# Kernel tuning notes

Measured on AMD Instinct MI355X. Metric: run time of the kernel, lower is better.

Reference implementation:

```python
import jax, jax.numpy as jnp
import numpy as np

B, L, D, H, DH, DEPTH, VOCAB = 8, 512, 256, 8, 64, 16, 5
INNER = 4 * D  # GLU feedforward inner dim = 1024
EPS = 1e-5

def _ln(x, g, b):
    mu = jnp.mean(x, -1, keepdims=True)
    var = jnp.mean(jnp.square(x - mu), -1, keepdims=True)
    return (x - mu) * jax.lax.rsqrt(var + EPS) * g + b

def setup_inputs() -> dict:
    key = jax.random.key(0)
    ks = jax.random.split(key, 24)
    s = 0.02
    seq = jax.random.randint(ks[0], (B, L), 0, VOCAB)
    lengths = jax.random.randint(ks[1], (B,), L // 2, L + 1)
    mask = jnp.arange(L)[None, :] < lengths[:, None]  # [B, L] bool padding mask
    f32 = jnp.float32
    return {
        "seq": seq,
        "mask": mask,
        "emb": jax.random.normal(ks[2], (VOCAB, D), f32) * s,
        "png": jnp.ones((D,), f32), "pnb": jnp.zeros((D,), f32),
        "ln1g": jnp.ones((DEPTH, D), f32), "ln1b": jnp.zeros((DEPTH, D), f32),
        "Wq": jax.random.normal(ks[3], (DEPTH, D, H * DH), f32) * s,
        "Wk": jax.random.normal(ks[4], (DEPTH, D, H * DH), f32) * s,
        "Wv": jax.random.normal(ks[5], (DEPTH, D, H * DH), f32) * s,
        "Wo": jax.random.normal(ks[6], (DEPTH, H * DH, D), f32) * s,
        "ln2g": jnp.ones((DEPTH, D), f32), "ln2b": jnp.zeros((DEPTH, D), f32),
        "W1": jax.random.normal(ks[7], (DEPTH, D, 2 * INNER), f32) * s,
        "b1": jnp.zeros((DEPTH, 2 * INNER), f32),
        "W2": jax.random.normal(ks[8], (DEPTH, INNER, D), f32) * s,
        "b2": jnp.zeros((DEPTH, D), f32),
        "fng": jnp.ones((D,), f32), "fnb": jnp.zeros((D,), f32),
        "Wout": jax.random.normal(ks[9], (D, 2), f32) * s,
        "bout": jnp.zeros((2,), f32),
    }

def _alibi_bias(n):
    # heads=8 is a power of two: slopes = 2^{-1}..2^{-8}
    slopes = 2.0 ** (-(jnp.arange(1, H + 1, dtype=jnp.float32)) * (8.0 / H))
    pos = jnp.arange(n, dtype=jnp.float32)
    rel = -jnp.abs(pos[None, :] - pos[:, None])  # [n, n]
    return slopes[:, None, None] * rel  # [H, n, n]

def _forward(seq, mask, emb, png, pnb, ln1g, ln1b, Wq, Wk, Wv, Wo,
             ln2g, ln2b, W1, b1, W2, b2, fng, fnb, Wout, bout):
    x = emb[seq]                      # [B, L, D]
    x = _ln(x, png, pnb)              # post_emb_norm
    bias = _alibi_bias(L)             # [H, L, L]
    kv_mask = mask[:, None, None, :]  # [B, 1, 1, L]
    scale = DH ** -0.5

    def layer(x, p):
        (g1, c1, wq, wk, wv, wo, g2, c2, w1, bb1, w2, bb2) = p
        h = _ln(x, g1, c1)
        q = (h @ wq).reshape(B, L, H, DH).transpose(0, 2, 1, 3)  # bhld
        k = (h @ wk).reshape(B, L, H, DH).transpose(0, 2, 1, 3)
        v = (h @ wv).reshape(B, L, H, DH).transpose(0, 2, 1, 3)
        scores = jnp.einsum('bhid,bhjd->bhij', q, k) * scale + bias
        scores = jnp.where(kv_mask, scores, jnp.float32(-1e9))
        a = jax.nn.softmax(scores, axis=-1)
        o = jnp.einsum('bhij,bhjd->bhid', a, v)
        o = o.transpose(0, 2, 1, 3).reshape(B, L, H * DH) @ wo
        x = x + o
        h2 = _ln(x, g2, c2)
        u = h2 @ w1 + bb1
        val, gate = jnp.split(u, 2, axis=-1)  # GLU: x * gelu(gate)
        x = x + (val * jax.nn.gelu(gate, approximate=False)) @ w2 + bb2
        return x, None

    x, _ = jax.lax.scan(layer, x, (ln1g, ln1b, Wq, Wk, Wv, Wo, ln2g, ln2b, W1, b1, W2, b2))
    x = _ln(x, fng, fnb)              # final encoder norm
    return x @ Wout + bout            # [B, L, 2]

def reference(seq, mask, emb, png, pnb, ln1g, ln1b, Wq, Wk, Wv, Wo,
              ln2g, ln2b, W1, b1, W2, b2, fng, fnb, Wout, bout):
    return _forward(seq, mask, emb, png, pnb, ln1g, ln1b, Wq, Wk, Wv, Wo,
                    ln2g, ln2b, W1, b1, W2, b2, fng, fnb, Wout, bout)
```

## Files before the change

kernel.cpp:

```cpp
#include <hip/hip_runtime.h>
#include <cstdint>
#include <cstddef>

#define BB 8
#define LL 512
#define DD 256
#define HH 8
#define DHD 64
#define NLAYER 16
#define HDH 512
#define IN2 2048
#define IN1 1024

typedef __attribute__((ext_vector_type(8))) short short8;
typedef __attribute__((ext_vector_type(4))) float floatx4;
typedef __attribute__((ext_vector_type(4))) unsigned short ushort4v;
typedef unsigned short u16;

__device__ __forceinline__ floatx4 mfma16(short8 a, short8 b, floatx4 c) {
  return __builtin_amdgcn_mfma_f32_16x16x32_bf16(a, b, c, 0, 0, 0);
}

__device__ __forceinline__ u16 f2b(float f) {
  union { float f; unsigned u; } x; x.f = f;
  unsigned u = x.u + 0x7fffu + ((x.u >> 16) & 1u);
  return (u16)(u >> 16);
}
__device__ __forceinline__ float b2f(u16 s) {
  union { unsigned u; float f; } x; x.u = ((unsigned)s) << 16;
  return x.f;
}

__device__ __forceinline__ float wave_sum(float s) {
#pragma unroll
  for (int off = 32; off; off >>= 1) s += __shfl_xor(s, off);
  return s;
}

__device__ __forceinline__ void gload_lds16(const u16* g, u16* l) {
  __builtin_amdgcn_global_load_lds((__attribute__((address_space(1))) void*)g,
                                   (__attribute__((address_space(3))) void*)l,
                                   16, 0, 0);
}

template <int NSLOTS, int NTHREADS = 256>
__device__ __forceinline__ void stage_tile(const u16* __restrict__ g, int rowstride,
                                           u16* lds, int tid) {
  int wave = tid >> 6, lane = tid & 63;
#pragma unroll
  for (int j = 0; j < NSLOTS / NTHREADS; ++j) {
    int sbase = j * NTHREADS + wave * 64;
    int slot = sbase + lane;
    int row = slot >> 3;
    int kg = (slot & 7) ^ (row & 7);
    gload_lds16(g + (size_t)row * rowstride + kg * 8, lds + sbase * 8);
  }
}

__device__ __forceinline__ short8 ld_frag(const u16* T, int row, int kg) {
  return *(const short8*)&T[(row << 6) + (((kg ^ row) & 7) << 3)];
}

__device__ __forceinline__ float4 ln_math(const float* __restrict__ x,
                                          const float* __restrict__ g,
                                          const float* __restrict__ b, int t) {
  float4 v = *(const float4*)(x + t * 4);
  float s = wave_sum(v.x + v.y + v.z + v.w);
  float mu = s * (1.0f / DD);
  float dx = v.x - mu, dy = v.y - mu, dz = v.z - mu, dw = v.w - mu;
  float ss = wave_sum(dx * dx + dy * dy + dz * dz + dw * dw);
  float r = rsqrtf(ss * (1.0f / DD) + 1e-5f);
  float4 gg = *(const float4*)(g + t * 4);
  float4 bb = *(const float4*)(b + t * 4);
  float4 o;
  o.x = dx * r * gg.x + bb.x;
  o.y = dy * r * gg.y + bb.y;
  o.z = dz * r * gg.z + bb.z;
  o.w = dw * r * gg.w + bb.w;
  return o;
}

__global__ __launch_bounds__(256) void embed_ln_kernel(
    const int* __restrict__ seq, const float* __restrict__ emb,
    const float* __restrict__ png, const float* __restrict__ pnb,
    const float* __restrict__ g1, const float* __restrict__ b1,
    float* __restrict__ X, u16* __restrict__ H) {
  int row = blockIdx.x * 4 + (threadIdx.x >> 6), t = threadIdx.x & 63;
  int tok = seq[row];
  float4 o = ln_math(emb + (size_t)tok * DD, png, pnb, t);
  *(float4*)(X + (size_t)row * DD + t * 4) = o;
  float s = wave_sum(o.x + o.y + o.z + o.w);
  float mu = s * (1.0f / DD);
  float dx = o.x - mu, dy = o.y - mu, dz = o.z - mu, dw = o.w - mu;
  float ss = wave_sum(dx * dx + dy * dy + dz * dz + dw * dw);
  float r = rsqrtf(ss * (1.0f / DD) + 1e-5f);
  float4 gg = *(const float4*)(g1 + t * 4);
  float4 bb = *(const float4*)(b1 + t * 4);
  ushort4v o4;
  o4[0] = f2b(dx * r * gg.x + bb.x);
  o4[1] = f2b(dy * r * gg.y + bb.y);
  o4[2] = f2b(dz * r * gg.z + bb.z);
  o4[3] = f2b(dw * r * gg.w + bb.w);
  *(ushort4v*)(H + (size_t)row * DD + t * 4) = o4;
}

#define WBUF_LAYER 1310720
__global__ __launch_bounds__(256) void prep_weights_kernel(
    const float* __restrict__ Wq, const float* __restrict__ Wk,
    const float* __restrict__ Wv, const float* __restrict__ Wo,
    const float* __restrict__ W1, const float* __restrict__ W2,
    u16* __restrict__ wbuf_all) {
  __shared__ float tile[32][33];
  int l = blockIdx.x / 1280;
  int bx = blockIdx.x % 1280;
  int tid = threadIdx.x;
  const float* wq = Wq + (size_t)l * DD * HDH;
  const float* wk = Wk + (size_t)l * DD * HDH;
  const float* wv = Wv + (size_t)l * DD * HDH;
  const float* wo = Wo + (size_t)l * HDH * DD;
  const float* w1 = W1 + (size_t)l * DD * IN2;
  const float* w2 = W2 + (size_t)l * IN1 * DD;
  u16* wbuf = wbuf_all + (size_t)l * WBUF_LAYER;

  const float* src; int srcld; u16* dst; int dstld; int dn0, k0, scol0;
  int packW1 = 0;
  if (bx < 384) {
    int t = bx; dn0 = (t % 48) * 32; k0 = (t / 48) * 32;
    scol0 = dn0 & 511;
    src = (dn0 < 512) ? wq : ((dn0 < 1024) ? wk : wv);
    srcld = 512; dst = wbuf; dstld = 256;
  } else if (bx < 512) {
    int t = bx - 384; dn0 = (t % 8) * 32; k0 = (t / 8) * 32; scol0 = dn0;
    src = wo; srcld = 256; dst = wbuf + 393216; dstld = 512;
  } else if (bx < 1024) {
    int t = bx - 512; dn0 = (t % 64) * 32; k0 = (t / 64) * 32; scol0 = dn0;
    src = w1; srcld = 2048; dst = wbuf + 524288; dstld = 256; packW1 = 1;
  } else {
    int t = bx - 1024; dn0 = (t % 8) * 32; k0 = (t / 8) * 32; scol0 = dn0;
    src = w2; srcld = 256; dst = wbuf + 1048576; dstld = 1024;
  }
  int r = tid >> 3, c4 = (tid & 7) * 4;
  float4 v = *(const float4*)&src[(size_t)(k0 + r) * srcld + scol0 + c4];
  tile[r][c4 + 0] = v.x; tile[r][c4 + 1] = v.y;
  tile[r][c4 + 2] = v.z; tile[r][c4 + 3] = v.w;
  __syncthreads();
  int n = tid >> 3, kk = (tid & 7) * 4;
  int drow = dn0 + n;
  if (packW1) {
    if (drow < 1024) drow = ((drow >> 4) << 5) | (drow & 15);
    else { int nn = drow - 1024; drow = (((nn >> 4) << 5) + 16) | (nn & 15); }
  }
  ushort4v o4;
  o4[0] = f2b(tile[kk + 0][n]); o4[1] = f2b(tile[kk + 1][n]);
  o4[2] = f2b(tile[kk + 2][n]); o4[3] = f2b(tile[kk + 3][n]);
  *(ushort4v*)&dst[(size_t)drow * dstld + k0 + kk] = o4;
}

__global__ __launch_bounds__(256) void gemm_qkv(
    const u16* __restrict__ A, const u16* __restrict__ BT,
    u16* __restrict__ qk, u16* __restrict__ vT) {
  __shared__ __align__(16) u16 As[2][128 * 64];
  __shared__ __align__(16) u16 Bs[2][128 * 64];
  int tid = threadIdx.x;
  int wave = tid >> 6, lane = tid & 63;
  int lm = lane & 15, quad = lane >> 4;
  int wr = wave >> 1, wc = wave & 1;
  int n0 = blockIdx.x * 128, m0 = blockIdx.y * 128;
  const u16* Ab = A + (size_t)m0 * DD;
  const u16* Bb = BT + (size_t)n0 * DD;

  floatx4 acc[4][4];
#pragma unroll
  for (int mf = 0; mf < 4; ++mf)
#pragma unroll
    for (int nf = 0; nf < 4; ++nf)
#pragma unroll
      for (int r = 0; r < 4; ++r) acc[mf][nf][r] = 0.0f;

  stage_tile<1024>(Ab, DD, As[0], tid);
  stage_tile<1024>(Bb, DD, Bs[0], tid);
  __syncthreads();
#pragma unroll
  for (int it = 0; it < 4; ++it) {
    if (it < 3) {
      stage_tile<1024>(Ab + (it + 1) * 64, DD, As[(it + 1) & 1], tid);
      stage_tile<1024>(Bb + (it + 1) * 64, DD, Bs[(it + 1) & 1], tid);
    }
    const u16* Ac = As[it & 1];
    const u16* Bc = Bs[it & 1];
#pragma unroll
    for (int kc = 0; kc < 2; ++kc) {
      short8 af[4], bf[4];
#pragma unroll
      for (int mf = 0; mf < 4; ++mf)
        af[mf] = ld_frag(Ac, wr * 64 + mf * 16 + lm, kc * 4 + quad);
#pragma unroll
      for (int nf = 0; nf < 4; ++nf)
        bf[nf] = ld_frag(Bc, wc * 64 + nf * 16 + lm, kc * 4 + quad);
#pragma unroll
      for (int mf = 0; mf < 4; ++mf)
#pragma unroll
        for (int nf = 0; nf < 4; ++nf)
          acc[mf][nf] = mfma16(af[mf], bf[nf], acc[mf][nf]);
    }
    if (it < 3) __syncthreads();
  }
  if (n0 < 1024) {
#pragma unroll
    for (int mf = 0; mf < 4; ++mf)
#pragma unroll
      for (int nf = 0; nf < 4; ++nf)
#pragma unroll
        for (int r = 0; r < 4; ++r) {
          int row = m0 + wr * 64 + mf * 16 + quad * 4 + r;
          int col = n0 + wc * 64 + nf * 16 + lm;
          qk[(size_t)row * 1024 + col] = f2b(acc[mf][nf][r]);
        }
  } else {
#pragma unroll
    for (int mf = 0; mf < 4; ++mf)
#pragma unroll
      for (int nf = 0; nf < 4; ++nf) {
        int token0 = m0 + wr * 64 + mf * 16 + quad * 4;
        int hd = n0 + wc * 64 + nf * 16 + lm - 1024;
        int b = token0 >> 9, key = token0 & 511;
        ushort4v p4;
#pragma unroll
        for (int r = 0; r < 4; ++r) p4[r] = f2b(acc[mf][nf][r]);
        *(ushort4v*)&vT[((size_t)(b * 8 + (hd >> 6)) * 64 + (hd & 63)) * 512 + key] = p4;
      }
  }
}

__global__ __launch_bounds__(256) void gemm_ffn1(
    const u16* __restrict__ A, const u16* __restrict__ BTp,
    const float* __restrict__ b1, u16* __restrict__ G) {
  __shared__ __align__(16) u16 As[2][128 * 64];
  __shared__ __align__(16) u16 Bs[2][128 * 64];
  int tid = threadIdx.x;
  int wave = tid >> 6, lane = tid & 63;
  int lm = lane & 15, quad = lane >> 4;
  int wr = wave >> 1, wc = wave & 1;
  int n0 = blockIdx.x * 128, m0 = blockIdx.y * 128;
  const u16* Ab = A + (size_t)m0 * DD;
  const u16* Bb = BTp + (size_t)n0 * DD;

  floatx4 acc[4][4];
#pragma unroll
  for (int mf = 0; mf < 4; ++mf)
#pragma unroll
    for (int nf = 0; nf < 4; ++nf)
#pragma unroll
      for (int r = 0; r < 4; ++r) acc[mf][nf][r] = 0.0f;

  stage_tile<1024>(Ab, DD, As[0], tid);
  stage_tile<1024>(Bb, DD, Bs[0], tid);
  __syncthreads();
#pragma unroll
  for (int it = 0; it < 4; ++it) {
    if (it < 3) {
      stage_tile<1024>(Ab + (it + 1) * 64, DD, As[(it + 1) & 1], tid);
      stage_tile<1024>(Bb + (it + 1) * 64, DD, Bs[(it + 1) & 1], tid);
    }
    const u16* Ac = As[it & 1];
    const u16* Bc = Bs[it & 1];
#pragma unroll
    for (int kc = 0; kc < 2; ++kc) {
      short8 af[4], bf[4];
#pragma unroll
      for (int mf = 0; mf < 4; ++mf)
        af[mf] = ld_frag(Ac, wr * 64 + mf * 16 + lm, kc * 4 + quad);
#pragma unroll
      for (int nf = 0; nf < 4; ++nf)
        bf[nf] = ld_frag(Bc, wc * 64 + nf * 16 + lm, kc * 4 + quad);
#pragma unroll
      for (int mf = 0; mf < 4; ++mf)
#pragma unroll
        for (int nf = 0; nf < 4; ++nf)
          acc[mf][nf] = mfma16(af[mf], bf[nf], acc[mf][nf]);
    }
    if (it < 3) __syncthreads();
  }
  int p0 = (n0 + wc * 64) >> 5;
#pragma unroll
  for (int j = 0; j < 2; ++j) {
    int gcol = (p0 + j) * 16 + lm;
    float bv = b1[gcol], bg = b1[1024 + gcol];
#pragma unroll
    for (int mf = 0; mf < 4; ++mf)
#pragma unroll
      for (int r = 0; r < 4; ++r) {
        int row = m0 + wr * 64 + mf * 16 + quad * 4 + r;
        float val = acc[mf][2 * j][r] + bv;
        float gate = acc[mf][2 * j + 1][r] + bg;
        float ge = 0.5f * gate * (1.0f + erff(gate * 0.70710678118654752440f));
        G[(size_t)row * IN1 + gcol] = f2b(val * ge);
      }
  }
}

__global__ __launch_bounds__(512) void gemm_row_ln(
    const u16* __restrict__ A, int lda, const u16* __restrict__ BT, int K,
    const float* __restrict__ bias, float* __restrict__ X,
    const float* __restrict__ lng, const float* __restrict__ lnb,
    u16* __restrict__ Hout,
    const float* __restrict__ Wout, const float* __restrict__ bout,
    float* __restrict__ outp) {
  __shared__ __align__(16) u16 As[2][16 * 64];
  __shared__ __align__(16) u16 Bs[2][256 * 64];
  int tid = threadIdx.x;
  int wave = tid >> 6, lane = tid & 63;
  int lm = lane & 15, quad = lane >> 4;
  int m0 = blockIdx.x * 16;

  floatx4 acc[2];
#pragma unroll
  for (int nf = 0; nf < 2; ++nf)
#pragma unroll
    for (int r = 0; r < 4; ++r) acc[nf][r] = 0.0f;

  const u16* Ab = A + (size_t)m0 * lda;
  if (wave < 2) {
    int slot = wave * 64 + lane;
    int row = slot >> 3, kg = (slot & 7) ^ (row & 7);
    gload_lds16(Ab + (size_t)row * lda + kg * 8, As[0] + wave * 64 * 8);
  }
  stage_tile<2048, 512>(BT, K, Bs[0], tid);
  __syncthreads();
  int iters = K >> 6;
  for (int it = 0; it < iters; ++it) {
    if (it + 1 < iters) {
      int kn = (it + 1) * 64;
      if (wave < 2) {
        int slot = wave * 64 + lane;
        int row = slot >> 3, kg = (slot & 7) ^ (row & 7);
        gload_lds16(Ab + (size_t)row * lda + kn + kg * 8,
                    As[(it + 1) & 1] + wave * 64 * 8);
      }
      stage_tile<2048, 512>(BT + kn, K, Bs[(it + 1) & 1], tid);
    }
    const u16* Ac = As[it & 1];
    const u16* Bc = Bs[it & 1];
#pragma unroll
    for (int kc = 0; kc < 2; ++kc) {
      short8 af = ld_frag(Ac, lm, kc * 4 + quad);
#pragma unroll
      for (int nf = 0; nf < 2; ++nf) {
        short8 bf = ld_frag(Bc, wave * 32 + nf * 16 + lm, kc * 4 + quad);
        acc[nf] = mfma16(af, bf, acc[nf]);
      }
    }
    if (it + 1 < iters) __syncthreads();
  }
  float* xs = (float*)Bs[0];
#pragma unroll
  for (int nf = 0; nf < 2; ++nf) {
    int col = wave * 32 + nf * 16 + lm;
    float bv = bias ? bias[col] : 0.0f;
#pragma unroll
    for (int r = 0; r < 4; ++r) {
      int row = quad * 4 + r;
      float v = acc[nf][r] + bv + X[(size_t)(m0 + row) * DD + col];
      X[(size_t)(m0 + row) * DD + col] = v;
      xs[row * DD + col] = v;
    }
  }
  __syncthreads();
  float4 gg = *(const float4*)(lng + lane * 4);
  float4 bb = *(const float4*)(lnb + lane * 4);
#pragma unroll
  for (int rr = 0; rr < 2; ++rr) {
    int row = wave * 2 + rr;
    float4 v = *(const float4*)&xs[row * DD + lane * 4];
    float s = wave_sum(v.x + v.y + v.z + v.w);
    float mu = s * (1.0f / DD);
    float dx = v.x - mu, dy = v.y - mu, dz = v.z - mu, dw = v.w - mu;
    float ss = wave_sum(dx * dx + dy * dy + dz * dz + dw * dw);
    float rc = rsqrtf(ss * (1.0f / DD) + 1e-5f);
    float o0 = dx * rc * gg.x + bb.x;
    float o1 = dy * rc * gg.y + bb.y;
    float o2 = dz * rc * gg.z + bb.z;
    float o3 = dw * rc * gg.w + bb.w;
    ushort4v o4;
    o4[0] = f2b(o0); o4[1] = f2b(o1); o4[2] = f2b(o2); o4[3] = f2b(o3);
    *(ushort4v*)(Hout + (size_t)(m0 + row) * DD + lane * 4) = o4;
    if (Wout) {
      int d0 = lane * 4;
      float s0 = o0 * Wout[d0 * 2] + o1 * Wout[(d0 + 1) * 2] +
                 o2 * Wout[(d0 + 2) * 2] + o3 * Wout[(d0 + 3) * 2];
      float s1 = o0 * Wout[d0 * 2 + 1] + o1 * Wout[(d0 + 1) * 2 + 1] +
                 o2 * Wout[(d0 + 2) * 2 + 1] + o3 * Wout[(d0 + 3) * 2 + 1];
      s0 = wave_sum(s0);
      s1 = wave_sum(s1);
      if (lane == 0) {
        outp[(size_t)(m0 + row) * 2 + 0] = s0 + bout[0];
        outp[(size_t)(m0 + row) * 2 + 1] = s1 + bout[1];
      }
    }
  }
}

__global__ __launch_bounds__(256) void attn_mfma_kernel(
    const u16* __restrict__ qk, const u16* __restrict__ vT,
    const int* __restrict__ mask_raw, u16* __restrict__ O) {
  __shared__ __align__(16) u16 Ks[2][64 * 64];
  __shared__ __align__(16) u16 Vs[2][64 * 64];
  __shared__ __align__(16) u16 Ps[4][16][72];
  __shared__ __align__(16) float madd[64];

  const int tid = threadIdx.x, wave = tid >> 6, lane = tid & 63;
  const int lm = lane & 15, quad = lane >> 4;
  const int qb = blockIdx.x, h = blockIdx.y, b = blockIdx.z;
  const float slope = exp2f(-(float)(h + 1));

  int w0 = mask_raw[0];
  int mmode = (w0 == 1) ? 0 : ((w0 == 0x3f800000) ? 2 : 1);
  const int krow_base = b * LL;

  int ntv = 8;
#pragma unroll
  for (int t = 7; t >= 0; --t) {
    bool tv;
    int gi = krow_base + t * 64;
    if (mmode == 0) tv = mask_raw[gi] != 0;
    else if (mmode == 1) tv = ((const signed char*)mask_raw)[gi] != 0;
    else tv = ((const float*)mask_raw)[gi] != 0.0f;
    if (!tv) ntv = t;
  }

  const int q0 = qb * 64 + wave * 16;
  const int qg = b * LL + q0;
  const float qpos = (float)(q0 + lm);

  const u16* qp = qk + (size_t)(qg + lm) * 1024 + h * 64 + quad * 8;
  short8 qf0 = *(const short8*)qp;
  short8 qf1 = *(const short8*)(qp + 32);

  floatx4 oc[4];
#pragma unroll
  for (int nf = 0; nf < 4; ++nf)
#pragma unroll
    for (int r = 0; r < 4; ++r) oc[nf][r] = 0.0f;
  float mrow = -1e30f, lrow = 0.0f;

  const u16* kbase_p = qk + (size_t)krow_base * 1024 + 512 + h * 64;
  const u16* vbase = vT + (size_t)(b * 8 + h) * 64 * 512;

  stage_tile<512>(kbase_p, 1024, Ks[0], tid);
  stage_tile<512>(vbase, 512, Vs[0], tid);
  if (tid < 64) {
    int gi = krow_base + (ntv - 1) * 64 + tid;
    bool valid;
    if (mmode == 0) valid = mask_raw[gi] != 0;
    else if (mmode == 1) valid = ((const signed char*)mask_raw)[gi] != 0;
    else valid = ((const float*)mask_raw)[gi] != 0.0f;
    madd[tid] = valid ? 0.0f : -1e9f;
  }
  __syncthreads();

  for (int t = 0; t < ntv; ++t) {
    int k0 = t * 64;
    if (t + 1 < ntv) {
      stage_tile<512>(kbase_p + (size_t)(t + 1) * 64 * 1024, 1024, Ks[(t + 1) & 1], tid);
      stage_tile<512>(vbase + (t + 1) * 64, 512, Vs[(t + 1) & 1], tid);
    }
    const u16* Kc = Ks[t & 1];
    const u16* Vc = Vs[t & 1];
    bool bnd = (t == ntv - 1);

    float sc[4][4];
    float tmax = -3e38f;
#pragma unroll
    for (int nt = 0; nt < 4; ++nt) {
      floatx4 pc;
#pragma unroll
      for (int r = 0; r < 4; ++r) pc[r] = 0.0f;
      short8 kf0 = ld_frag(Kc, nt * 16 + lm, quad);
      short8 kf1 = ld_frag(Kc, nt * 16 + lm, 4 + quad);
      pc = mfma16(kf0, qf0, pc);
      pc = mfma16(kf1, qf1, pc);
      float kbase = (float)(k0 + nt * 16 + quad * 4);
#pragma unroll
      for (int r = 0; r < 4; ++r) {
        float s = pc[r] * 0.125f - slope * fabsf(qpos - (kbase + r));
        sc[nt][r] = s;
      }
      if (bnd) {
        float4 ma = *(const float4*)&madd[nt * 16 + quad * 4];
#pragma unroll
        for (int r = 0; r < 4; ++r) sc[nt][r] += ((const float*)&ma)[r];
      }
#pragma unroll
      for (int r = 0; r < 4; ++r) tmax = fmaxf(tmax, sc[nt][r]);
    }
    tmax = fmaxf(tmax, __shfl_xor(tmax, 16));
    tmax = fmaxf(tmax, __shfl_xor(tmax, 32));
    float nm = fmaxf(mrow, tmax);
    float alpha = __expf(mrow - nm);
    mrow = nm;
    float rsum = 0.0f;
#pragma unroll
    for (int nt = 0; nt < 4; ++nt)
#pragma unroll
      for (int r = 0; r < 4; ++r) {
        float p = __expf(sc[nt][r] - nm);
        sc[nt][r] = p;
        rsum += p;
      }
    rsum += __shfl_xor(rsum, 16);
    rsum += __shfl_xor(rsum, 32);
    lrow = lrow * alpha + rsum;
    float av[4];
#pragma unroll
    for (int r = 0; r < 4; ++r) av[r] = __shfl(alpha, quad * 4 + r);
#pragma unroll
    for (int nf = 0; nf < 4; ++nf)
#pragma unroll
      for (int r = 0; r < 4; ++r) oc[nf][r] *= av[r];
#pragma unroll
    for (int nt = 0; nt < 4; ++nt) {
      ushort4v p4;
#pragma unroll
      for (int r = 0; r < 4; ++r) p4[r] = f2b(sc[nt][r]);
      *(ushort4v*)&Ps[wave][lm][nt * 16 + quad * 4] = p4;
    }
#pragma unroll
    for (int kc = 0; kc < 2; ++kc) {
      short8 af = *(const short8*)&Ps[wave][lm][kc * 32 + quad * 8];
#pragma unroll
      for (int nf = 0; nf < 4; ++nf) {
        short8 bv = ld_frag(Vc, nf * 16 + lm, kc * 4 + quad);
        oc[nf] = mfma16(af, bv, oc[nf]);
      }
    }
    if (t + 1 < ntv) __syncthreads();
  }
  float rl = 1.0f / lrow;
  float rv[4];
#pragma unroll
  for (int r = 0; r < 4; ++r) rv[r] = __shfl(rl, quad * 4 + r);
#pragma unroll
  for (int nf = 0; nf < 4; ++nf)
#pragma unroll
    for (int r = 0; r < 4; ++r) {
      int qq = qg + quad * 4 + r;
      O[(size_t)qq * HDH + h * 64 + nf * 16 + lm] = f2b(oc[nf][r] * rv[r]);
    }
}

extern "C" void kernel_launch(void* const* d_in, const int* in_sizes, int n_in,
                              void* d_out, int out_size, void* d_ws, size_t ws_size,
                              hipStream_t stream) {
  const int* seq = (const int*)d_in[0];
  const int* mask = (const int*)d_in[1];
  const float* emb = (const float*)d_in[2];
  const float* png = (const float*)d_in[3];
  const float* pnb = (const float*)d_in[4];
  const float* ln1g = (const float*)d_in[5];
  const float* ln1b = (const float*)d_in[6];
  const float* Wq = (const float*)d_in[7];
  const float* Wk = (const float*)d_in[8];
  const float* Wv = (const float*)d_in[9];
  const float* Wo = (const float*)d_in[10];
  const float* ln2g = (const float*)d_in[11];
  const float* ln2b = (const float*)d_in[12];
  const float* W1 = (const float*)d_in[13];
  const float* b1 = (const float*)d_in[14];
  const float* W2 = (const float*)d_in[15];
  const float* b2 = (const float*)d_in[16];
  const float* fng = (const float*)d_in[17];
  const float* fnb = (const float*)d_in[18];
  const float* Wout = (const float*)d_in[19];
  const float* bout = (const float*)d_in[20];
  float* out = (float*)d_out;

  uint8_t* wsb = (uint8_t*)d_ws;
  float* x = (float*)(wsb + 0);
  u16* hb = (u16*)(wsb + 4194304);
  u16* wbuf = (u16*)(wsb + 6291456);
  u16* qk = (u16*)(wsb + 48234496);
  u16* vT = (u16*)(wsb + 56623104);
  u16* obuf = (u16*)(wsb + 60817408);
  u16* gbuf = (u16*)(wsb + 65011712);

  const int M = BB * LL;

  prep_weights_kernel<<<16 * 1280, 256, 0, stream>>>(Wq, Wk, Wv, Wo, W1, W2, wbuf);
  embed_ln_kernel<<<M / 4, 256, 0, stream>>>(seq, emb, png, pnb, ln1g, ln1b, x, hb);

  for (int l = 0; l < NLAYER; ++l) {
    u16* wl = wbuf + (size_t)l * WBUF_LAYER;

    gemm_qkv<<<dim3(1536 / 128, M / 128), 256, 0, stream>>>(hb, wl, qk, vT);

    attn_mfma_kernel<<<dim3(LL / 64, HH, BB), 256, 0, stream>>>(qk, vT, mask, obuf);

    gemm_row_ln<<<M / 16, 512, 0, stream>>>(
        obuf, HDH, wl + 393216, HDH, nullptr, x,
        ln2g + l * DD, ln2b + l * DD, hb, nullptr, nullptr, nullptr);

    gemm_ffn1<<<dim3(IN2 / 128, M / 128), 256, 0, stream>>>(
        hb, wl + 524288, b1 + (size_t)l * IN2, gbuf);

    const float* ng = (l < NLAYER - 1) ? (ln1g + (l + 1) * DD) : fng;
    const float* nb = (l < NLAYER - 1) ? (ln1b + (l + 1) * DD) : fnb;
    const float* wo_p = (l == NLAYER - 1) ? Wout : nullptr;
    const float* bo_p = (l == NLAYER - 1) ? bout : nullptr;
    float* out_p = (l == NLAYER - 1) ? out : nullptr;
    gemm_row_ln<<<M / 16, 512, 0, stream>>>(
        gbuf, IN1, wl + 1048576, IN1, b2 + (size_t)l * DD, x, ng, nb, hb,
        wo_p, bo_p, out_p);
  }

  (void)in_sizes; (void)n_in; (void)out_size; (void)ws_size;
}
```

Before: 1.280 ms.

## Retile QKV GEMM, widen row-LN K-step, double attention query block

The QKV GEMM now uses 96-column tiles, which yields 16x32 blocks instead of 12x32 to fill more CUs. Its epilogue picks the qk or vT store per fragment. The row-LN GEMM stages 128-wide K chunks with a new 16-group swizzle, which halves the number of iterations and barriers at the cost of doubling LDS use. The attention kernel runs 8 waves over 128 queries per block, so each staged K/V tile is shared by twice as many queries, but there are half as many blocks.

New measurement: 1.223 ms. 1.05x faster.

```diff
diff --git a/kernel.cpp b/kernel.cpp
--- a/kernel.cpp
+++ b/kernel.cpp
@@ -59,6 +59,11 @@
 
 __device__ __forceinline__ short8 ld_frag(const u16* T, int row, int kg) {
   return *(const short8*)&T[(row << 6) + (((kg ^ row) & 7) << 3)];
+}
+
+__device__ __forceinline__ short8 ld_frag128(const u16* T, int row, int kg) {
+  int pg = (kg & 8) | ((kg ^ row) & 7);
+  return *(const short8*)&T[(row << 7) + (pg << 3)];
 }
 
 __device__ __forceinline__ float4 ln_math(const float* __restrict__ x,
@@ -160,76 +165,72 @@
     const u16* __restrict__ A, const u16* __restrict__ BT,
     u16* __restrict__ qk, u16* __restrict__ vT) {
   __shared__ __align__(16) u16 As[2][128 * 64];
-  __shared__ __align__(16) u16 Bs[2][128 * 64];
+  __shared__ __align__(16) u16 Bs[2][96 * 64];
   int tid = threadIdx.x;
   int wave = tid >> 6, lane = tid & 63;
   int lm = lane & 15, quad = lane >> 4;
   int wr = wave >> 1, wc = wave & 1;
-  int n0 = blockIdx.x * 128, m0 = blockIdx.y * 128;
+  int n0 = blockIdx.x * 96, m0 = blockIdx.y * 128;
   const u16* Ab = A + (size_t)m0 * DD;
   const u16* Bb = BT + (size_t)n0 * DD;
 
-  floatx4 acc[4][4];
+  floatx4 acc[4][3];
 #pragma unroll
   for (int mf = 0; mf < 4; ++mf)
 #pragma unroll
-    for (int nf = 0; nf < 4; ++nf)
+    for (int nf = 0; nf < 3; ++nf)
 #pragma unroll
       for (int r = 0; r < 4; ++r) acc[mf][nf][r] = 0.0f;
 
   stage_tile<1024>(Ab, DD, As[0], tid);
-  stage_tile<1024>(Bb, DD, Bs[0], tid);
+  stage_tile<768>(Bb, DD, Bs[0], tid);
   __syncthreads();
 #pragma unroll
   for (int it = 0; it < 4; ++it) {
     if (it < 3) {
       stage_tile<1024>(Ab + (it + 1) * 64, DD, As[(it + 1) & 1], tid);
-      stage_tile<1024>(Bb + (it + 1) * 64, DD, Bs[(it + 1) & 1], tid);
+      stage_tile<768>(Bb + (it + 1) * 64, DD, Bs[(it + 1) & 1], tid);
     }
     const u16* Ac = As[it & 1];
     const u16* Bc = Bs[it & 1];
 #pragma unroll
     for (int kc = 0; kc < 2; ++kc) {
-      short8 af[4], bf[4];
+      short8 af[4], bf[3];
 #pragma unroll
       for (int mf = 0; mf < 4; ++mf)
         af[mf] = ld_frag(Ac, wr * 64 + mf * 16 + lm, kc * 4 + quad);
 #pragma unroll
-      for (int nf = 0; nf < 4; ++nf)
-        bf[nf] = ld_frag(Bc, wc * 64 + nf * 16 + lm, kc * 4 + quad);
+      for (int nf = 0; nf < 3; ++nf)
+        bf[nf] = ld_frag(Bc, wc * 48 + nf * 16 + lm, kc * 4 + quad);
 #pragma unroll
       for (int mf = 0; mf < 4; ++mf)
 #pragma unroll
-        for (int nf = 0; nf < 4; ++nf)
+        for (int nf = 0; nf < 3; ++nf)
           acc[mf][nf] = mfma16(af[mf], bf[nf], acc[mf][nf]);
     }
     if (it < 3) __syncthreads();
   }
-  if (n0 < 1024) {
-#pragma unroll
-    for (int mf = 0; mf < 4; ++mf)
-#pragma unroll
-      for (int nf = 0; nf < 4; ++nf)
+#pragma unroll
+  for (int mf = 0; mf < 4; ++mf)
+#pragma unroll
+    for (int nf = 0; nf < 3; ++nf) {
+      int colf = n0 + wc * 48 + nf * 16;
+      if (colf < 1024) {
 #pragma unroll
         for (int r = 0; r < 4; ++r) {
           int row = m0 + wr * 64 + mf * 16 + quad * 4 + r;
-          int col = n0 + wc * 64 + nf * 16 + lm;
-          qk[(size_t)row * 1024 + col] = f2b(acc[mf][nf][r]);
+          qk[(size_t)row * 1024 + colf + lm] = f2b(acc[mf][nf][r]);
         }
-  } else {
-#pragma unroll
-    for (int mf = 0; mf < 4; ++mf)
-#pragma unroll
-      for (int nf = 0; nf < 4; ++nf) {
+      } else {
         int token0 = m0 + wr * 64 + mf * 16 + quad * 4;
-        int hd = n0 + wc * 64 + nf * 16 + lm - 1024;
+        int hd = colf + lm - 1024;
         int b = token0 >> 9, key = token0 & 511;
         ushort4v p4;
 #pragma unroll
         for (int r = 0; r < 4; ++r) p4[r] = f2b(acc[mf][nf][r]);
         *(ushort4v*)&vT[((size_t)(b * 8 + (hd >> 6)) * 64 + (hd & 63)) * 512 + key] = p4;
       }
-  }
+    }
 }
 
 __global__ __launch_bounds__(256) void gemm_ffn1(
@@ -306,8 +307,8 @@
     u16* __restrict__ Hout,
     const float* __restrict__ Wout, const float* __restrict__ bout,
     float* __restrict__ outp) {
-  __shared__ __align__(16) u16 As[2][16 * 64];
-  __shared__ __align__(16) u16 Bs[2][256 * 64];
+  __shared__ __align__(16) u16 As[2][16 * 128];
+  __shared__ __align__(16) u16 Bs[2][256 * 128];
   int tid = threadIdx.x;
   int wave = tid >> 6, lane = tid & 63;
   int lm = lane & 15, quad = lane >> 4;
@@ -320,38 +321,50 @@
     for (int r = 0; r < 4; ++r) acc[nf][r] = 0.0f;
 
   const u16* Ab = A + (size_t)m0 * lda;
-  if (wave < 2) {
-    int slot = wave * 64 + lane;
-    int row = slot >> 3, kg = (slot & 7) ^ (row & 7);
-    gload_lds16(Ab + (size_t)row * lda + kg * 8, As[0] + wave * 64 * 8);
-  }
-  stage_tile<2048, 512>(BT, K, Bs[0], tid);
+
+  auto stageA = [&](int k0, u16* dst) {
+    if (wave < 4) {
+      int sbase = wave * 64;
+      int slot = sbase + lane;
+      int row = slot >> 4, pg = slot & 15;
+      int kg = (pg & 8) | ((pg ^ row) & 7);
+      gload_lds16(Ab + (size_t)row * lda + k0 + kg * 8, dst + sbase * 8);
+    }
+  };
+  auto stageB = [&](int k0, u16* dst) {
+#pragma unroll
+    for (int j = 0; j < 8; ++j) {
+      int sbase = j * 512 + wave * 64;
+      int slot = sbase + lane;
+      int row = slot >> 4, pg = slot & 15;
+      int kg = (pg & 8) | ((pg ^ row) & 7);
+      gload_lds16(BT + (size_t)row * K + k0 + kg * 8, dst + sbase * 8);
+    }
+  };
+
+  stageA(0, As[0]);
+  stageB(0, Bs[0]);
   __syncthreads();
-  int iters = K >> 6;
+  int iters = K >> 7;
   for (int it = 0; it < iters; ++it) {
     if (it + 1 < iters) {
-      int kn = (it + 1) * 64;
-      if (wave < 2) {
-        int slot = wave * 64 + lane;
-        int row = slot >> 3, kg = (slot & 7) ^ (row & 7);
-        gload_lds16(Ab + (size_t)row * lda + kn + kg * 8,
-                    As[(it + 1) & 1] + wave * 64 * 8);
-      }
-      stage_tile<2048, 512>(BT + kn, K, Bs[(it + 1) & 1], tid);
+      stageA((it + 1) * 128, As[(it + 1) & 1]);
+      stageB((it + 1) * 128, Bs[(it + 1) & 1]);
     }
     const u16* Ac = As[it & 1];
     const u16* Bc = Bs[it & 1];
 #pragma unroll
-    for (int kc = 0; kc < 2; ++kc) {
-      short8 af = ld_frag(Ac, lm, kc * 4 + quad);
+    for (int kc = 0; kc < 4; ++kc) {
+      short8 af = ld_frag128(Ac, lm, kc * 4 + quad);
 #pragma unroll
       for (int nf = 0; nf < 2; ++nf) {
-        short8 bf = ld_frag(Bc, wave * 32 + nf * 16 + lm, kc * 4 + quad);
+        short8 bf = ld_frag128(Bc, wave * 32 + nf * 16 + lm, kc * 4 + quad);
         acc[nf] = mfma16(af, bf, acc[nf]);
       }
     }
     if (it + 1 < iters) __syncthreads();
   }
+  __syncthreads();
   float* xs = (float*)Bs[0];
 #pragma unroll
   for (int nf = 0; nf < 2; ++nf) {
@@ -400,12 +413,12 @@
   }
 }
 
-__global__ __launch_bounds__(256) void attn_mfma_kernel(
+__global__ __launch_bounds__(512) void attn_mfma_kernel(
     const u16* __restrict__ qk, const u16* __restrict__ vT,
     const int* __restrict__ mask_raw, u16* __restrict__ O) {
   __shared__ __align__(16) u16 Ks[2][64 * 64];
   __shared__ __align__(16) u16 Vs[2][64 * 64];
-  __shared__ __align__(16) u16 Ps[4][16][72];
+  __shared__ __align__(16) u16 Ps[8][16][72];
   __shared__ __align__(16) float madd[64];
 
   const int tid = threadIdx.x, wave = tid >> 6, lane = tid & 63;
@@ -428,7 +441,7 @@
     if (!tv) ntv = t;
   }
 
-  const int q0 = qb * 64 + wave * 16;
+  const int q0 = qb * 128 + wave * 16;
   const int qg = b * LL + q0;
   const float qpos = (float)(q0 + lm);
 
@@ -446,8 +459,8 @@
   const u16* kbase_p = qk + (size_t)krow_base * 1024 + 512 + h * 64;
   const u16* vbase = vT + (size_t)(b * 8 + h) * 64 * 512;
 
-  stage_tile<512>(kbase_p, 1024, Ks[0], tid);
-  stage_tile<512>(vbase, 512, Vs[0], tid);
+  stage_tile<512, 512>(kbase_p, 1024, Ks[0], tid);
+  stage_tile<512, 512>(vbase, 512, Vs[0], tid);
   if (tid < 64) {
     int gi = krow_base + (ntv - 1) * 64 + tid;
     bool valid;
@@ -461,8 +474,9 @@
   for (int t = 0; t < ntv; ++t) {
     int k0 = t * 64;
     if (t + 1 < ntv) {
-      stage_tile<512>(kbase_p + (size_t)(t + 1) * 64 * 1024, 1024, Ks[(t + 1) & 1], tid);
-      stage_tile<512>(vbase + (t + 1) * 64, 512, Vs[(t + 1) & 1], tid);
+      stage_tile<512, 512>(kbase_p + (size_t)(t + 1) * 64 * 1024, 1024,
+                           Ks[(t + 1) & 1], tid);
+      stage_tile<512, 512>(vbase + (t + 1) * 64, 512, Vs[(t + 1) & 1], tid);
     }
     const u16* Kc = Ks[t & 1];
     const u16* Vc = Vs[t & 1];
@@ -591,9 +605,9 @@
   for (int l = 0; l < NLAYER; ++l) {
     u16* wl = wbuf + (size_t)l * WBUF_LAYER;
 
-    gemm_qkv<<<dim3(1536 / 128, M / 128), 256, 0, stream>>>(hb, wl, qk, vT);
-
-    attn_mfma_kernel<<<dim3(LL / 64, HH, BB), 256, 0, stream>>>(qk, vT, mask, obuf);
+    gemm_qkv<<<dim3(1536 / 96, M / 128), 256, 0, stream>>>(hb, wl, qk, vT);
+
+    attn_mfma_kernel<<<dim3(LL / 128, HH, BB), 512, 0, stream>>>(qk, vT, mask, obuf);
 
     gemm_row_ln<<<M / 16, 512, 0, stream>>>(
         obuf, HDH, wl + 393216, HDH, nullptr, x,
```
